# Performance work log

Measured on AMD Instinct MI355X. Metric: run time of the kernel, lower is better.

Reference implementation:

```python
import jax, jax.numpy as jnp
import numpy as np

B, L, D, H, FF, K = 2, 2048, 1024, 16, 4096, 5
HD = D // H
EPS = 1e-5

def _rope_matrix():
    pos = jnp.arange(L, dtype=jnp.float32)
    inv = 1.0 / (10000.0 ** (jnp.arange(0, HD, 2, dtype=jnp.float32) / HD))
    ang = pos[:, None] * inv[None, :]                       # [L, HD//2]
    # buffer layout matches torch: cat([cos, sin], -1) -> [1,1,L,HD]
    return jnp.concatenate([jnp.cos(ang), jnp.sin(ang)], -1)[None, None]

def _alibi():
    i = jnp.arange(L)
    dist = jnp.clip(i[:, None] - i[None, :], 0, None).astype(jnp.float32)
    slopes = 2.0 ** (-(2.0 ** (-(np.log2(H) - 3.0))) * jnp.arange(H, dtype=jnp.float32))
    return slopes[:, None, None] * dist                     # [H,L,L]

def _apply_rope(x, pe):
    # faithful even/odd slicing of the concatenated [cos|sin] buffer
    xe, xo = x[..., ::2], x[..., 1::2]
    c, s = pe[..., ::2], pe[..., 1::2]
    return jnp.concatenate([xe * c - xo * s, xe * s + xo * c], -1)

def _ln(x, g, b):
    m = x.mean(-1, keepdims=True)
    v = ((x - m) ** 2).mean(-1, keepdims=True)
    return (x - m) * jax.lax.rsqrt(v + EPS) * g + b

def _attn(x, wq, bq, wk, bk, wv, bv, wo, bo, pe, alibi):
    q = (x @ wq + bq).reshape(B, L, H, HD).transpose(0, 2, 1, 3)
    k = (x @ wk + bk).reshape(B, L, H, HD).transpose(0, 2, 1, 3)
    v = (x @ wv + bv).reshape(B, L, H, HD).transpose(0, 2, 1, 3)
    q = _apply_rope(q, pe)
    k = _apply_rope(k, pe)
    scores = jnp.einsum('bhqd,bhkd->bhqk', q, k) * (HD ** -0.5) + alibi[None]
    w = jax.nn.softmax(scores, axis=-1)
    o = jnp.einsum('bhqk,bhkd->bhqd', w, v).transpose(0, 2, 1, 3).reshape(B, L, D)
    return o @ wo + bo

def _conv_block(x, g, b, pw1_w, pw1_b, dw_w, dw_b, bn_g, bn_b, pw2_w, pw2_b):
    res = x
    h = _ln(x, g, b)
    h = h @ pw1_w + pw1_b                                   # pointwise 1: [B,L,2D]
    h = h[..., :D] * jax.nn.sigmoid(h[..., D:])             # GLU -> [B,L,D]
    h = h.transpose(0, 2, 1)                                # [B,D,L]
    w = dw_w[:, None, ::-1]                                 # ConvTranspose1d(stride=1,pad=K//2) == corr with flipped kernel
    h = jax.lax.conv_general_dilated(h, w, (1,), [(K // 2, K // 2)],
        dimension_numbers=('NCH', 'OIH', 'NCH'), feature_group_count=D)
    h = h + dw_b[None, :, None]
    h = h * jax.lax.rsqrt(jnp.float32(1.0 + EPS)) * bn_g[None, :, None] + bn_b[None, :, None]  # eval BN
    h = h * jax.nn.relu6(h + 3.0) / 6.0                     # hardswish
    h = h.transpose(0, 2, 1) @ pw2_w + pw2_b                # pointwise 2: [B,L,D]
    return h + res[:, :1, :]                                # Upsample(size=1) residual (nearest -> t=0)

def reference(memory, wq, bq, wk, bk, wv, bv, wo, bo, n1_g, n1_b,
              cln_g, cln_b, pw1_w, pw1_b, dw_w, dw_b, bn_g, bn_b, pw2_w, pw2_b,
              proj_w, proj_b, proj2_w, proj2_b, lin1_w, lin1_b, lin2_w, lin2_b,
              n3_g, n3_b):
    pe = _rope_matrix()
    alibi = _alibi()
    tgt2 = _attn(memory, wq, bq, wk, bk, wv, bv, wo, bo, pe, alibi)
    memory = memory + _ln(tgt2, n1_g, n1_b)
    conv = _conv_block(memory, cln_g, cln_b, pw1_w, pw1_b, dw_w, dw_b,
                       bn_g, bn_b, pw2_w, pw2_b)
    proj = jnp.einsum('bld,lm->bmd', memory, proj_w) + proj_b[:, None]   # Linear over seq axis
    proj = proj @ proj2_w + proj2_b
    memory = proj + conv
    tgt2 = jax.nn.gelu(memory @ lin1_w + lin1_b, approximate=False) @ lin2_w + lin2_b
    return _ln(memory + tgt2, n3_g, n3_b)

def setup_inputs():
    ks = iter(jax.random.split(jax.random.key(0), 48))
    def w(shape, s=0.02):
        return jax.random.normal(next(ks), shape, dtype=jnp.float32) * s
    z = lambda *s: jnp.zeros(s, dtype=jnp.float32)
    o = lambda *s: jnp.ones(s, dtype=jnp.float32)
    return {
        'memory': jax.random.normal(next(ks), (B, L, D), dtype=jnp.float32),
        'wq': w((D, D)), 'bq': z(D), 'wk': w((D, D)), 'bk': z(D),
        'wv': w((D, D)), 'bv': z(D), 'wo': w((D, D)), 'bo': z(D),
        'n1_g': o(D), 'n1_b': z(D),
        'cln_g': o(D), 'cln_b': z(D),
        'pw1_w': w((D, 2 * D)), 'pw1_b': z(2 * D),
        'dw_w': w((D, K), 0.1), 'dw_b': z(D),
        'bn_g': o(D), 'bn_b': z(D),
        'pw2_w': w((D, D)), 'pw2_b': z(D),
        'proj_w': w((L, L)), 'proj_b': z(L),
        'proj2_w': w((D, D)), 'proj2_b': z(D),
        'lin1_w': w((D, FF)), 'lin1_b': z(FF),
        'lin2_w': w((FF, D)), 'lin2_b': z(D),
        'n3_g': o(D), 'n3_b': z(D),
    }
```

## Files before the change

### kernel.cpp

```cpp
#include <hip/hip_runtime.h>
#include <hip/hip_bf16.h>
#include <math.h>

constexpr int Bc = 2, Lc = 2048, Dc = 1024, Hc = 16, HDc = 64, FFc = 4096;
constexpr int NT = Bc * Lc;
constexpr size_t TD = (size_t)NT * Dc;
constexpr size_t MEG = 1024 * 1024;

__device__ __forceinline__ float ldf(const float* p) { return *p; }
__device__ __forceinline__ unsigned short f2b(float f) {
  __hip_bfloat16 h = __float2bfloat16(f);
  return *reinterpret_cast<unsigned short*>(&h);
}

using frag   = __attribute__((ext_vector_type(8))) short;
using f32x4v = __attribute__((ext_vector_type(4))) float;

__device__ __forceinline__ void async16(const unsigned short* g, unsigned short* l) {
  __builtin_amdgcn_global_load_lds(
      (const __attribute__((address_space(1))) unsigned int*)g,
      (__attribute__((address_space(3))) unsigned int*)l, 16, 0, 0);
}

__device__ __forceinline__ float block_sum(float v, float* red) {
  const int lane = threadIdx.x & 63, w = threadIdx.x >> 6;
  #pragma unroll
  for (int o = 32; o > 0; o >>= 1) v += __shfl_down(v, o, 64);
  __syncthreads();
  if (lane == 0) red[w] = v;
  __syncthreads();
  return red[0] + red[1] + red[2] + red[3];
}

__global__ __launch_bounds__(256)
void convert_bf16_kernel(const float* __restrict__ IN, unsigned short* __restrict__ OUT)
{
  const size_t gid = (size_t)blockIdx.x * 256 + threadIdx.x;
  const float4 v = *(const float4*)(IN + gid * 4);
  ushort4 o;
  o.x = f2b(v.x); o.y = f2b(v.y); o.z = f2b(v.z); o.w = f2b(v.w);
  *(ushort4*)(OUT + gid * 4) = o;
}

__global__ __launch_bounds__(256)
void transpose_convert_kernel(const float* __restrict__ IN, unsigned short* __restrict__ OUT,
                              int R, int C, long long sIn, long long sOut)
{
  __shared__ float tile[64][65];
  const int t = threadIdx.x;
  const float* in = IN + (long long)blockIdx.z * sIn;
  unsigned short* out = OUT + (long long)blockIdx.z * sOut;
  const int r0 = blockIdx.y * 64, c0 = blockIdx.x * 64;
  #pragma unroll
  for (int i = 0; i < 4; i++) {
    const int r = (t >> 4) + i * 16, c4 = (t & 15) * 4;
    const float4 v = *(const float4*)(in + (size_t)(r0 + r) * C + c0 + c4);
    tile[r][c4+0] = v.x; tile[r][c4+1] = v.y; tile[r][c4+2] = v.z; tile[r][c4+3] = v.w;
  }
  __syncthreads();
  #pragma unroll
  for (int i = 0; i < 4; i++) {
    const int cc = (t >> 4) + i * 16, rr4 = (t & 15) * 4;
    ushort4 o;
    o.x = f2b(tile[rr4+0][cc]); o.y = f2b(tile[rr4+1][cc]);
    o.z = f2b(tile[rr4+2][cc]); o.w = f2b(tile[rr4+3][cc]);
    *(ushort4*)(out + (size_t)(c0 + cc) * R + r0 + rr4) = o;
  }
}

struct TPack {
  const float* in[10]; unsigned short* out[10];
  int R[10], C[10], tx[10], start[10];
};
__global__ __launch_bounds__(256)
void fused_transpose_kernel(TPack p)
{
  __shared__ float tile[64][65];
  const int bid = blockIdx.x;
  int s = 0;
  #pragma unroll
  for (int i = 1; i < 10; i++) s = (bid >= p.start[i]) ? i : s;
  const float* in = p.in[s];
  unsigned short* out = p.out[s];
  const int R = p.R[s], C = p.C[s];
  const int local = bid - p.start[s];
  const int bx = local % p.tx[s], by = local / p.tx[s];
  const int r0 = by * 64, c0 = bx * 64;
  const int t = threadIdx.x;
  #pragma unroll
  for (int i = 0; i < 4; i++) {
    const int r = (t >> 4) + i * 16, c4 = (t & 15) * 4;
    const float4 v = *(const float4*)(in + (size_t)(r0 + r) * C + c0 + c4);
    tile[r][c4+0] = v.x; tile[r][c4+1] = v.y; tile[r][c4+2] = v.z; tile[r][c4+3] = v.w;
  }
  __syncthreads();
  #pragma unroll
  for (int i = 0; i < 4; i++) {
    const int cc = (t >> 4) + i * 16, rr4 = (t & 15) * 4;
    ushort4 o;
    o.x = f2b(tile[rr4+0][cc]); o.y = f2b(tile[rr4+1][cc]);
    o.z = f2b(tile[rr4+2][cc]); o.w = f2b(tile[rr4+3][cc]);
    *(ushort4*)(out + (size_t)(c0 + cc) * R + r0 + rr4) = o;
  }
}

constexpr int EPI_BIAS = 0, EPI_BIAS_ROW = 1, EPI_GELU = 2, EPI_ADD = 3, EPI_ADDROW0 = 4,
              EPI_QKV = 5;

template<int BM, int EPI, bool OUTBF, bool OUTBOTH>
__global__ __launch_bounds__(256)
void mfma_gemm_kernel(const unsigned short* __restrict__ A, const unsigned short* __restrict__ Bt,
                      const float* __restrict__ bias, const float* __restrict__ bias2,
                      const float* __restrict__ bias3, const float* __restrict__ extra,
                      float* __restrict__ C, unsigned short* __restrict__ Cbf,
                      int M, int N, int K,
                      long long sA, long long sB, long long sC)
{
  constexpr int NTt = (BM == 128) ? 4 : 2;
  __shared__ unsigned short As[2][BM][4][8];
  __shared__ unsigned short Bs[2][128][4][8];
  const int tid = threadIdx.x;
  const int l = tid & 63, w = tid >> 6;
  const int wm = (BM == 128) ? (w & 1) * 64 : 0;
  const int wn = (BM == 128) ? (w >> 1) * 64 : w * 32;
  const int m0 = blockIdx.y * BM, n0 = blockIdx.x * 128;
  const unsigned short* Ap = A + (long long)blockIdx.z * sA;
  const unsigned short* Bp = Bt + (long long)blockIdx.z * sB;

  f32x4v acc[4][NTt];
  #pragma unroll
  for (int mt = 0; mt < 4; mt++)
    #pragma unroll
    for (int nt = 0; nt < NTt; nt++) acc[mt][nt] = {0.f, 0.f, 0.f, 0.f};

  const int c_ = l >> 4, rm = l & 15;
  int rrB[2], ggB[2];
  #pragma unroll
  for (int j = 0; j < 2; j++) {
    const int chunk = w * 128 + j * 64 + l;
    rrB[j] = chunk >> 2;
    ggB[j] = (chunk & 3) ^ ((rrB[j] >> 1) & 3);
  }
  int rrA = 0, ggA = 0;
  if constexpr (BM == 64) {
    const int chunkA = w * 64 + l;
    rrA = chunkA >> 2;
    ggA = (chunkA & 3) ^ ((rrA >> 1) & 3);
  }

  auto stage = [&](int bi, int k0) {
    if constexpr (BM == 128) {
      #pragma unroll
      for (int j = 0; j < 2; j++) {
        async16(Ap + (size_t)(m0 + rrB[j]) * K + k0 + ggB[j] * 8,
                &As[bi][0][0][0] + (size_t)(w * 128 + j * 64) * 8);
        async16(Bp + (size_t)(n0 + rrB[j]) * K + k0 + ggB[j] * 8,
                &Bs[bi][0][0][0] + (size_t)(w * 128 + j * 64) * 8);
      }
    } else {
      async16(Ap + (size_t)(m0 + rrA) * K + k0 + ggA * 8,
              &As[bi][0][0][0] + (size_t)(w * 64) * 8);
      #pragma unroll
      for (int j = 0; j < 2; j++)
        async16(Bp + (size_t)(n0 + rrB[j]) * K + k0 + ggB[j] * 8,
                &Bs[bi][0][0][0] + (size_t)(w * 128 + j * 64) * 8);
    }
  };

  stage(0, 0);
  __syncthreads();
  int cur = 0;
  const int sg = (rm >> 1) & 3;

  for (int k0 = 0; k0 < K; k0 += 32) {
    if (k0 + 32 < K) stage(cur ^ 1, k0 + 32);

    frag af[4], bfr[NTt];
    #pragma unroll
    for (int mt = 0; mt < 4; mt++)
      af[mt] = *(const frag*)&As[cur][wm + mt * 16 + rm][c_ ^ sg][0];
    #pragma unroll
    for (int nt = 0; nt < NTt; nt++)
      bfr[nt] = *(const frag*)&Bs[cur][wn + nt * 16 + rm][c_ ^ sg][0];
    #pragma unroll
    for (int mt = 0; mt < 4; mt++)
      #pragma unroll
      for (int nt = 0; nt < NTt; nt++)
        acc[mt][nt] = __builtin_amdgcn_mfma_f32_16x16x32_bf16(af[mt], bfr[nt], acc[mt][nt], 0, 0, 0);

    __syncthreads();
    cur ^= 1;
  }

  float* Cp = C + (long long)blockIdx.z * sC;
  unsigned short* Cbp = Cbf + (long long)blockIdx.z * sC;
  #pragma unroll
  for (int mt = 0; mt < 4; mt++) {
    #pragma unroll
    for (int nt = 0; nt < NTt; nt++) {
      const int mq = m0 + wm + mt * 16 + c_ * 4;
      const int n  = n0 + wn + nt * 16 + rm;
      if constexpr (EPI == EPI_QKV) {
        const float* bp = (n < 1024) ? bias : ((n < 2048) ? bias2 : bias3);
        const float bv_ = ldf(bp + (n & 1023));
        const float r0 = acc[mt][nt][0] + bv_;
        const float r1 = acc[mt][nt][1] + bv_;
        const float r2 = acc[mt][nt][2] + bv_;
        const float r3 = acc[mt][nt][3] + bv_;
        if (n < 2048) {
          float* dst = Cp + (size_t)(n >> 10) * TD + (size_t)mq * Dc + (n & 1023);
          dst[0] = r0; dst[Dc] = r1; dst[2 * Dc] = r2; dst[3 * Dc] = r3;
        } else {
          ushort4 o;
          o.x = f2b(r0); o.y = f2b(r1); o.z = f2b(r2); o.w = f2b(r3);
          *(ushort4*)(Cbp + (size_t)(mq >> 11) * ((size_t)Lc * Dc)
                      + (size_t)(n - 2048) * Lc + (mq & (Lc - 1))) = o;
        }
      } else {
        #pragma unroll
        for (int i = 0; i < 4; i++) {
          const int m = mq + i;
          float r = acc[mt][nt][i];
          if constexpr (EPI == EPI_BIAS || EPI == EPI_GELU || EPI == EPI_ADD || EPI == EPI_ADDROW0)
            r += ldf(bias + n);
          if constexpr (EPI == EPI_BIAS_ROW) r += ldf(bias + m);
          if constexpr (EPI == EPI_GELU)
            r = 0.5f * r * (1.0f + erff(r * 0.70710678118654752f));
          if constexpr (EPI == EPI_ADD) r += extra[(size_t)m * N + n];
          if constexpr (EPI == EPI_ADDROW0) r += extra[(size_t)(m >> 11) * ((size_t)Lc * Dc) + n];
          if constexpr (OUTBOTH) { Cp[(size_t)m * N + n] = r; Cbp[(size_t)m * N + n] = f2b(r); }
          else if constexpr (OUTBF) Cbp[(size_t)m * N + n] = f2b(r);
          else                      Cp[(size_t)m * N + n] = r;
        }
      }
    }
  }
}

__global__ __launch_bounds__(256)
void pe_fill_kernel(float* __restrict__ pet)
{
  const int gid = blockIdx.x * 256 + threadIdx.x;
  const int l = gid >> 6, t = gid & 63;
  const int j = t & 31;
  const float wj = exp2f(-(float)j * (13.2877123795494f / 32.0f));
  const float ang = (float)l * wj;
  pet[gid] = (t < 32) ? cosf(ang) : sinf(ang);
}

__global__ __launch_bounds__(256)
void rope2_kernel(const float* __restrict__ Qi, const float* __restrict__ Ki,
                  const float* __restrict__ pet,
                  unsigned short* __restrict__ Qo, unsigned short* __restrict__ Ko)
{
  int gid = blockIdx.x * 256 + threadIdx.x;
  const int sel = gid >= NT * Hc;
  if (sel) gid -= NT * Hc;
  const float* X = sel ? Ki : Qi;
  unsigned short* O = sel ? Ko : Qo;
  const float scl = sel ? 1.0f : 0.125f * 1.44269504f;
  const int h = gid & (Hc - 1);
  const int token = gid >> 4;
  const int l = token & (Lc - 1);
  const float* p = X + (size_t)token * Dc + h * HDc;
  unsigned short* po = O + (size_t)token * Dc + h * HDc;
  const float* pr = pet + l * 64;
  float x[64], out[64];
  #pragma unroll
  for (int i = 0; i < 16; i++) *(float4*)&x[4*i] = *(const float4*)&p[4*i];
  #pragma unroll
  for (int u = 0; u < 32; u++) {
    const int base = (u < 16) ? (2 * u) : (32 + 2 * (u - 16));
    const float c = pr[base], s = pr[base + 1];
    out[u]      = (x[2*u] * c - x[2*u+1] * s) * scl;
    out[32 + u] = (x[2*u] * s + x[2*u+1] * c) * scl;
  }
  #pragma unroll
  for (int i = 0; i < 16; i++) {
    ushort4 o;
    o.x = f2b(out[4*i+0]); o.y = f2b(out[4*i+1]);
    o.z = f2b(out[4*i+2]); o.w = f2b(out[4*i+3]);
    *(ushort4*)&po[4*i] = o;
  }
}

__global__ __launch_bounds__(256)
void flash_attn_mfma_kernel(const unsigned short* __restrict__ Q,
                            const unsigned short* __restrict__ K,
                            const unsigned short* __restrict__ VT,
                            unsigned short* __restrict__ O)
{
  __shared__ unsigned short Qs[64][8][8];
  __shared__ unsigned short Ks[2][64][8][8];
  __shared__ unsigned short Vt[2][64][8][8];
  __shared__ unsigned short Ps[64][72];
  const int tid = threadIdx.x;
  const int l = tid & 63, w = tid >> 6;
  const int lg = l >> 4, lm = l & 15;
  const int q0 = blockIdx.x * 64;
  const int bh = blockIdx.y;
  const int b = bh >> 4, h = bh & 15;
  const size_t rowbase = (size_t)b * Lc;
  const size_t vbase = (size_t)b * Lc * Dc;
  const int dbase = h * 64;
  const float sl2 = exp2f(-0.5f * (float)h) * 1.44269504f;

  auto stageKV = [&](int bi, int k0s) {
    #pragma unroll
    for (int j = 0; j < 2; j++) {
      const int chunk = (w * 2 + j) * 64 + l;
      const int r = chunk >> 3, gsrc = (chunk & 7) ^ (r & 7);
      async16(K + (rowbase + k0s + r) * Dc + dbase + gsrc * 8,
              &Ks[bi][0][0][0] + (size_t)chunk * 8);
      async16(VT + vbase + (size_t)(dbase + r) * Lc + k0s + gsrc * 8,
              &Vt[bi][0][0][0] + (size_t)chunk * 8);
    }
  };

  #pragma unroll
  for (int j = 0; j < 2; j++) {
    const int chunk = (w * 2 + j) * 64 + l;
    const int r = chunk >> 3, gsrc = (chunk & 7) ^ (r & 7);
    async16(Q + (rowbase + q0 + r) * Dc + dbase + gsrc * 8,
            &Qs[0][0][0] + (size_t)chunk * 8);
  }
  stageKV(0, 0);
  __syncthreads();
  frag qf[2];
  #pragma unroll
  for (int s = 0; s < 2; s++)
    qf[s] = *(const frag*)&Qs[w * 16 + lm][(s * 4 + lg) ^ (lm & 7)][0];

  const float qg = (float)(q0 + w * 16 + lm);
  float koff[4][4];
  #pragma unroll
  for (int kt = 0; kt < 4; kt++)
    #pragma unroll
    for (int i = 0; i < 4; i++) koff[kt][i] = (float)(kt * 16 + lg * 4 + i);

  float m_i = -3.0e38f, l_i = 0.f;
  f32x4v acc_o[4];
  #pragma unroll
  for (int dt = 0; dt < 4; dt++) acc_o[dt] = {0.f, 0.f, 0.f, 0.f};

  int cur = 0;
  for (int k0 = 0; k0 < Lc; k0 += 64) {
    if (k0 + 64 < Lc) stageKV(cur ^ 1, k0 + 64);

    f32x4v st[4];
    #pragma unroll
    for (int kt = 0; kt < 4; kt++) st[kt] = {0.f, 0.f, 0.f, 0.f};
    __builtin_amdgcn_s_setprio(1);
    #pragma unroll
    for (int kt = 0; kt < 4; kt++) {
      #pragma unroll
      for (int s = 0; s < 2; s++) {
        frag kf = *(const frag*)&Ks[cur][kt * 16 + lm][(s * 4 + lg) ^ (lm & 7)][0];
        st[kt] = __builtin_amdgcn_mfma_f32_16x16x32_bf16(kf, qf[s], st[kt], 0, 0, 0);
      }
    }
    __builtin_amdgcn_s_setprio(0);

    const float qk0 = qg - (float)k0;
    float sv[4][4], tmax = -3.0e38f;
    if (k0 + 64 <= q0) {
      #pragma unroll
      for (int kt = 0; kt < 4; kt++)
        #pragma unroll
        for (int i = 0; i < 4; i++) {
          const float v = fmaf(sl2, qk0 - koff[kt][i], st[kt][i]);
          sv[kt][i] = v; tmax = fmaxf(tmax, v);
        }
    } else if (k0 <= q0) {
      #pragma unroll
      for (int kt = 0; kt < 4; kt++)
        #pragma unroll
        for (int i = 0; i < 4; i++) {
          const float v = fmaf(sl2, fmaxf(qk0 - koff[kt][i], 0.f), st[kt][i]);
          sv[kt][i] = v; tmax = fmaxf(tmax, v);
        }
    } else {
      #pragma unroll
      for (int kt = 0; kt < 4; kt++)
        #pragma unroll
        for (int i = 0; i < 4; i++) {
          const float v = st[kt][i];
          sv[kt][i] = v; tmax = fmaxf(tmax, v);
        }
    }
    tmax = fmaxf(tmax, __shfl_xor(tmax, 16, 64));
    tmax = fmaxf(tmax, __shfl_xor(tmax, 32, 64));

    if (!__all(tmax < m_i - 27.0f)) {
      if (__any(tmax > m_i)) {
        const float mnew = fmaxf(m_i, tmax);
        const float alpha = exp2f(m_i - mnew);
        m_i = mnew;
        l_i *= alpha;
        float aO[4];
        #pragma unroll
        for (int i = 0; i < 4; i++) aO[i] = __shfl(alpha, lg * 4 + i, 64);
        #pragma unroll
        for (int dt = 0; dt < 4; dt++)
          #pragma unroll
          for (int i = 0; i < 4; i++) acc_o[dt][i] *= aO[i];
      }
      float rsum = 0.f;
      const int qrow = w * 16 + lm;
      #pragma unroll
      for (int kt = 0; kt < 4; kt++) {
        const float p0 = exp2f(sv[kt][0] - m_i), p1 = exp2f(sv[kt][1] - m_i);
        const float p2 = exp2f(sv[kt][2] - m_i), p3 = exp2f(sv[kt][3] - m_i);
        rsum += (p0 + p1) + (p2 + p3);
        ushort4 pk4;
        pk4.x = f2b(p0); pk4.y = f2b(p1); pk4.z = f2b(p2); pk4.w = f2b(p3);
        *(ushort4*)&Ps[qrow][kt * 16 + lg * 4] = pk4;
      }
      rsum += __shfl_xor(rsum, 16, 64);
      rsum += __shfl_xor(rsum, 32, 64);
      l_i += rsum;

      __builtin_amdgcn_s_setprio(1);
      #pragma unroll
      for (int c = 0; c < 2; c++) {
        frag ap = *(const frag*)&Ps[w * 16 + lm][c * 32 + lg * 8];
        #pragma unroll
        for (int dt = 0; dt < 4; dt++) {
          frag bv = *(const frag*)&Vt[cur][dt * 16 + lm][(c * 4 + lg) ^ (lm & 7)][0];
          acc_o[dt] = __builtin_amdgcn_mfma_f32_16x16x32_bf16(ap, bv, acc_o[dt], 0, 0, 0);
        }
      }
      __builtin_amdgcn_s_setprio(0);
    }

    __syncthreads();
    cur ^= 1;
  }

  float lO[4];
  #pragma unroll
  for (int i = 0; i < 4; i++) lO[i] = 1.0f / __shfl(l_i, lg * 4 + i, 64);
  #pragma unroll
  for (int dt = 0; dt < 4; dt++)
    #pragma unroll
    for (int i = 0; i < 4; i++)
      Ps[w * 16 + lg * 4 + i][dt * 16 + lm] = f2b(acc_o[dt][i] * lO[i]);
  __syncthreads();
  #pragma unroll
  for (int j = 0; j < 2; j++) {
    const int chunk = (w * 2 + j) * 64 + l;
    const int r = chunk >> 3, g = chunk & 7;
    alignas(16) unsigned short tmp[8];
    #pragma unroll
    for (int t = 0; t < 8; t++) tmp[t] = Ps[r][g * 8 + t];
    *(uint4*)(O + (rowbase + q0 + r) * Dc + dbase + g * 8) = *(uint4*)tmp;
  }
}

__global__ __launch_bounds__(256)
void ln_res_cln_kernel(const float* __restrict__ X, const float* __restrict__ RES,
                       const float* __restrict__ g1, const float* __restrict__ b1,
                       const float* __restrict__ g2, const float* __restrict__ b2,
                       float* __restrict__ OUT1, unsigned short* __restrict__ OUT2)
{
  __shared__ float red4[4];
  const int row = blockIdx.x, tid = threadIdx.x;
  const size_t base = (size_t)row * Dc + tid * 4;
  const float4 xv = *(const float4*)(X + base);
  float s = xv.x + xv.y + xv.z + xv.w;
  s = block_sum(s, red4);
  const float mean = s * (1.0f / Dc);
  const float d0 = xv.x-mean, d1 = xv.y-mean, d2 = xv.z-mean, d3 = xv.w-mean;
  float ss = d0*d0 + d1*d1 + d2*d2 + d3*d3;
  ss = block_sum(ss, red4);
  const float rstd = rsqrtf(ss * (1.0f / Dc) + 1e-5f);
  const int c = tid * 4;
  const float4 rv = *(const float4*)(RES + base);
  float y0 = rv.x + d0*rstd*ldf(g1+c+0) + ldf(b1+c+0);
  float y1 = rv.y + d1*rstd*ldf(g1+c+1) + ldf(b1+c+1);
  float y2 = rv.z + d2*rstd*ldf(g1+c+2) + ldf(b1+c+2);
  float y3 = rv.w + d3*rstd*ldf(g1+c+3) + ldf(b1+c+3);
  *(float4*)(OUT1 + base) = make_float4(y0, y1, y2, y3);
  float s2 = y0 + y1 + y2 + y3;
  s2 = block_sum(s2, red4);
  const float mean2 = s2 * (1.0f / Dc);
  const float e0 = y0-mean2, e1 = y1-mean2, e2 = y2-mean2, e3 = y3-mean2;
  float ss2 = e0*e0 + e1*e1 + e2*e2 + e3*e3;
  ss2 = block_sum(ss2, red4);
  const float rstd2 = rsqrtf(ss2 * (1.0f / Dc) + 1e-5f);
  ushort4 o;
  o.x = f2b(e0*rstd2*ldf(g2+c+0) + ldf(b2+c+0));
  o.y = f2b(e1*rstd2*ldf(g2+c+1) + ldf(b2+c+1));
  o.z = f2b(e2*rstd2*ldf(g2+c+2) + ldf(b2+c+2));
  o.w = f2b(e3*rstd2*ldf(g2+c+3) + ldf(b2+c+3));
  *(ushort4*)(OUT2 + base) = o;
}

__global__ __launch_bounds__(256)
void ln_sum_kernel(const float* __restrict__ X, const float* __restrict__ Y,
                   const float* __restrict__ g, const float* __restrict__ be,
                   float* __restrict__ OUT)
{
  __shared__ float red4[4];
  const int row = blockIdx.x, tid = threadIdx.x;
  const size_t base = (size_t)row * Dc + tid * 4;
  const float4 xv = *(const float4*)(X + base);
  const float4 yv = *(const float4*)(Y + base);
  const float x0 = xv.x+yv.x, x1 = xv.y+yv.y, x2 = xv.z+yv.z, x3 = xv.w+yv.w;
  float s = x0 + x1 + x2 + x3;
  s = block_sum(s, red4);
  const float mean = s * (1.0f / Dc);
  const float d0 = x0-mean, d1 = x1-mean, d2 = x2-mean, d3 = x3-mean;
  float ss = d0*d0 + d1*d1 + d2*d2 + d3*d3;
  ss = block_sum(ss, red4);
  const float rstd = rsqrtf(ss * (1.0f / Dc) + 1e-5f);
  const int c = tid * 4;
  float4 o;
  o.x = d0*rstd*ldf(g+c+0) + ldf(be+c+0);
  o.y = d1*rstd*ldf(g+c+1) + ldf(be+c+1);
  o.z = d2*rstd*ldf(g+c+2) + ldf(be+c+2);
  o.w = d3*rstd*ldf(g+c+3) + ldf(be+c+3);
  *(float4*)(OUT + base) = o;
}

__global__ __launch_bounds__(256)
void glu_kernel(const float* __restrict__ H1, float* __restrict__ HG)
{
  const int gid = blockIdx.x * 256 + threadIdx.x;
  const int t = gid >> 8;
  const int c4 = (gid & 255) * 4;
  const float* p = H1 + (size_t)t * (2 * Dc);
  const float4 a = *(const float4*)(p + c4);
  const float4 gg = *(const float4*)(p + Dc + c4);
  float4 o;
  o.x = a.x / (1.0f + expf(-gg.x));
  o.y = a.y / (1.0f + expf(-gg.y));
  o.z = a.z / (1.0f + expf(-gg.z));
  o.w = a.w / (1.0f + expf(-gg.w));
  *(float4*)(HG + (size_t)t * Dc + c4) = o;
}

__global__ __launch_bounds__(256)
void dwconv_bf16_kernel(const float* __restrict__ HG, const float* __restrict__ w,
                        const float* __restrict__ wb, const float* __restrict__ gn,
                        const float* __restrict__ bb, unsigned short* __restrict__ OUT)
{
  const int gid = blockIdx.x * 256 + threadIdx.x;
  const int d = gid & (Dc - 1);
  const int l = (gid >> 10) & (Lc - 1);
  const int b = gid >> 21;
  const size_t rowb = (size_t)b * Lc;
  float acc = ldf(wb + d);
  #pragma unroll
  for (int s = 0; s < 5; s++) {
    const int lp = l + 2 - s;
    if (lp >= 0 && lp < Lc)
      acc += ldf(w + d * 5 + s) * HG[((rowb + lp) << 10) + d];
  }
  const float rs = rsqrtf(1.0f + 1e-5f);
  const float t = acc * rs * ldf(gn + d) + ldf(bb + d);
  OUT[gid] = f2b(t * fminf(fmaxf(t + 3.0f, 0.0f), 6.0f) * (1.0f / 6.0f));
}

extern "C" void kernel_launch(void* const* d_in, const int* in_sizes, int n_in,
                              void* d_out, int out_size, void* d_ws, size_t ws_size,
                              hipStream_t stream) {
  (void)in_sizes; (void)n_in; (void)out_size; (void)ws_size;
  const float* mem    = (const float*)d_in[0];
  const float* wq     = (const float*)d_in[1];
  const float* bq     = (const float*)d_in[2];
  const float* wk     = (const float*)d_in[3];
  const float* bk     = (const float*)d_in[4];
  const float* wv     = (const float*)d_in[5];
  const float* bv     = (const float*)d_in[6];
  const float* wo     = (const float*)d_in[7];
  const float* bo     = (const float*)d_in[8];
  const float* n1g    = (const float*)d_in[9];
  const float* n1b    = (const float*)d_in[10];
  const float* clng   = (const float*)d_in[11];
  const float* clnb   = (const float*)d_in[12];
  const float* pw1w   = (const float*)d_in[13];
  const float* pw1b   = (const float*)d_in[14];
  const float* dww    = (const float*)d_in[15];
  const float* dwb    = (const float*)d_in[16];
  const float* bng    = (const float*)d_in[17];
  const float* bnb    = (const float*)d_in[18];
  const float* pw2w   = (const float*)d_in[19];
  const float* pw2b   = (const float*)d_in[20];
  const float* projw  = (const float*)d_in[21];
  const float* projb  = (const float*)d_in[22];
  const float* proj2w = (const float*)d_in[23];
  const float* proj2b = (const float*)d_in[24];
  const float* lin1w  = (const float*)d_in[25];
  const float* lin1b  = (const float*)d_in[26];
  const float* lin2w  = (const float*)d_in[27];
  const float* lin2b  = (const float*)d_in[28];
  const float* n3g    = (const float*)d_in[29];
  const float* n3b    = (const float*)d_in[30];
  float* out = (float*)d_out;

  char* base = (char*)d_ws;
  float* qb   = (float*)base;
  float* kb   = qb + TD;
  float* big1 = kb + TD;
  float* big2 = big1 + TD;
  float* ob   = big2 + TD;
  unsigned short* abf  = (unsigned short*)(base + 5 * TD * 4);
  unsigned short* qbf  = abf + TD;
  unsigned short* kbf  = qbf + TD;
  unsigned short* vtb  = kbf + TD;
  unsigned short* m1T  = vtb + TD;
  unsigned short* ffbbf= m1T + TD;
  unsigned short* wt   = ffbbf + 4 * TD;
  unsigned short* wqT    = wt;
  unsigned short* wkT    = wqT + MEG;
  unsigned short* wvT    = wkT + MEG;
  unsigned short* woT    = wvT + MEG;
  unsigned short* pw1T   = woT + MEG;
  unsigned short* pw2T   = pw1T + 2*MEG;
  unsigned short* proj2T = pw2T + MEG;
  unsigned short* projwT = proj2T + MEG;
  unsigned short* lin1T  = projwT + 4*MEG;
  unsigned short* lin2T  = lin1T + 4*MEG;
  float* pet = (float*)(lin2T + 4*MEG);

  const dim3 blk(256);
  const long long LD = (long long)Lc * Dc;

  TPack tp;
  const float* tin[10]  = {wq, wk, wv, wo, pw1w, pw2w, proj2w, projw, lin1w, lin2w};
  unsigned short* tout[10] = {wqT, wkT, wvT, woT, pw1T, pw2T, proj2T, projwT, lin1T, lin2T};
  const int tR[10] = {1024,1024,1024,1024,1024,1024,1024,2048,1024,4096};
  const int tC[10] = {1024,1024,1024,1024,2048,1024,1024,2048,4096,1024};
  int startAcc = 0;
  for (int i = 0; i < 10; i++) {
    tp.in[i] = tin[i]; tp.out[i] = tout[i];
    tp.R[i] = tR[i]; tp.C[i] = tC[i]; tp.tx[i] = tC[i] / 64;
    tp.start[i] = startAcc;
    startAcc += (tR[i] / 64) * (tC[i] / 64);
  }
  fused_transpose_kernel<<<dim3(startAcc), blk, 0, stream>>>(tp);
  pe_fill_kernel<<<dim3(Lc * 64 / 256), blk, 0, stream>>>(pet);

  convert_bf16_kernel<<<dim3((unsigned)(TD/1024)),blk,0,stream>>>(mem, abf);
  mfma_gemm_kernel<128,EPI_QKV,false,false><<<dim3(24,32,1),blk,0,stream>>>(
      abf, wqT, bq, bk, bv, nullptr, qb, vtb, NT, 3*Dc, Dc, 0, 0, 0);
  rope2_kernel<<<dim3(2*NT*Hc/256),blk,0,stream>>>(qb, kb, pet, qbf, kbf);
  flash_attn_mfma_kernel<<<dim3(Lc/64, Bc*Hc),blk,0,stream>>>(qbf,kbf,vtb,abf);
  mfma_gemm_kernel<64,EPI_BIAS,false,false><<<dim3(8,64,1),blk,0,stream>>>(
      abf,woT,bo,nullptr,nullptr,nullptr,qb,nullptr,NT,Dc,Dc,0,0,0);
  ln_res_cln_kernel<<<dim3(NT),blk,0,stream>>>(qb, mem, n1g, n1b, clng, clnb, kb, abf);

  mfma_gemm_kernel<128,EPI_BIAS,false,false><<<dim3(16,32,1),blk,0,stream>>>(
      abf,pw1T,pw1b,nullptr,nullptr,nullptr,big1,nullptr,NT,2*Dc,Dc,0,0,0);
  glu_kernel<<<dim3((unsigned)(TD/4/256)),blk,0,stream>>>(big1, ob);
  dwconv_bf16_kernel<<<dim3((unsigned)(TD/256)),blk,0,stream>>>(ob, dww, dwb, bng, bnb, abf);
  mfma_gemm_kernel<64,EPI_ADDROW0,false,false><<<dim3(8,64,1),blk,0,stream>>>(
      abf,pw2T,pw2b,nullptr,nullptr,kb,big2,nullptr,NT,Dc,Dc,0,0,0);

  transpose_convert_kernel<<<dim3(16,32,2),blk,0,stream>>>(kb, m1T, 2048, 1024, LD, LD);
  mfma_gemm_kernel<64,EPI_BIAS_ROW,true,false><<<dim3(8,32,2),blk,0,stream>>>(
      projwT,m1T,projb,nullptr,nullptr,nullptr,nullptr,abf,Lc,Dc,Lc,0,LD,LD);
  mfma_gemm_kernel<64,EPI_ADD,false,true><<<dim3(8,64,1),blk,0,stream>>>(
      abf,proj2T,proj2b,nullptr,nullptr,big2,big1,qbf,NT,Dc,Dc,0,0,0);

  mfma_gemm_kernel<128,EPI_GELU,true,false><<<dim3(32,32,1),blk,0,stream>>>(
      qbf,lin1T,lin1b,nullptr,nullptr,nullptr,nullptr,ffbbf,NT,FFc,Dc,0,0,0);
  mfma_gemm_kernel<64,EPI_BIAS,false,false><<<dim3(8,64,1),blk,0,stream>>>(
      ffbbf,lin2T,lin2b,nullptr,nullptr,nullptr,ob,nullptr,NT,Dc,FFc,0,0,0);

  ln_sum_kernel<<<dim3(NT),blk,0,stream>>>(big1, ob, n3g, n3b, out);
}
```

Baseline: 653.6 us.

## Skip loading K/V tiles whose Cauchy-Schwarz score bound cannot affect softmax

Adds a kernel that computes the maximum row L2 norm of each 64-row Q and K tile per head. The flash attention loop now uses the product of these norms plus the ALiBi bias maximum as an upper bound on tile scores. When that bound sits more than 27 (log2 units) below the current block-wide running max, it skips both the async K/V staging and the MFMA work for that tile. The P-to-bf16 conversion also switches to packed v_cvt_pk_bf16_f32 instructions. The bound is exact by Cauchy-Schwarz, but the skip only pays off when ALiBi makes far tiles negligible; it costs an extra kernel launch plus a per-iteration shared-memory min reduction.

```diff
diff --git a/kernel.cpp b/kernel.cpp
--- a/kernel.cpp
+++ b/kernel.cpp
@@ -285,15 +285,56 @@
 }
 
 __global__ __launch_bounds__(256)
+void tile_norm_kernel(const unsigned short* __restrict__ Qb,
+                      const unsigned short* __restrict__ Kb,
+                      float* __restrict__ qnb, float* __restrict__ knb)
+{
+  __shared__ float red[4];
+  const int tile = blockIdx.x, bh = blockIdx.y;
+  const int b = bh >> 4, h = bh & 15;
+  const unsigned short* X = blockIdx.z ? Qb : Kb;
+  const int tid = threadIdx.x;
+  const int row = tid >> 2, seg = tid & 3;
+  const unsigned short* p = X + ((size_t)(b * Lc + tile * 64 + row)) * Dc + h * 64 + seg * 16;
+  const uint4 v0 = *(const uint4*)p;
+  const uint4 v1 = *(const uint4*)(p + 8);
+  const unsigned int vv[8] = {v0.x, v0.y, v0.z, v0.w, v1.x, v1.y, v1.z, v1.w};
+  float ss = 0.f;
+  #pragma unroll
+  for (int i = 0; i < 8; i++) {
+    const float a = __uint_as_float(vv[i] << 16);
+    const float c = __uint_as_float(vv[i] & 0xffff0000u);
+    ss = fmaf(a, a, ss); ss = fmaf(c, c, ss);
+  }
+  ss += __shfl_xor(ss, 1, 64);
+  ss += __shfl_xor(ss, 2, 64);
+  float mx = ss;
+  mx = fmaxf(mx, __shfl_xor(mx, 4, 64));
+  mx = fmaxf(mx, __shfl_xor(mx, 8, 64));
+  mx = fmaxf(mx, __shfl_xor(mx, 16, 64));
+  mx = fmaxf(mx, __shfl_xor(mx, 32, 64));
+  if ((tid & 63) == 0) red[tid >> 6] = mx;
+  __syncthreads();
+  if (tid == 0) {
+    const float r = fmaxf(fmaxf(red[0], red[1]), fmaxf(red[2], red[3]));
+    (blockIdx.z ? qnb : knb)[bh * 32 + tile] = sqrtf(r);
+  }
+}
+
+__global__ __launch_bounds__(256)
 void flash_attn_mfma_kernel(const unsigned short* __restrict__ Q,
                             const unsigned short* __restrict__ K,
                             const unsigned short* __restrict__ VT,
+                            const float* __restrict__ qnb,
+                            const float* __restrict__ knb,
                             unsigned short* __restrict__ O)
 {
   __shared__ unsigned short Qs[64][8][8];
   __shared__ unsigned short Ks[2][64][8][8];
   __shared__ unsigned short Vt[2][64][8][8];
   __shared__ unsigned short Ps[64][72];
+  __shared__ float knS[32];
+  __shared__ float mS[64];
   const int tid = threadIdx.x;
   const int l = tid & 63, w = tid >> 6;
   const int lg = l >> 4, lm = l & 15;
@@ -325,6 +366,9 @@
             &Qs[0][0][0] + (size_t)chunk * 8);
   }
   stageKV(0, 0);
+  const float qmx = qnb[bh * 32 + blockIdx.x] * 1.01f;
+  if (tid < 32) knS[tid] = knb[bh * 32 + tid];
+  if (tid < 64) mS[tid] = -3.0e38f;
   __syncthreads();
   frag qf[2];
   #pragma unroll
@@ -343,98 +387,121 @@
   #pragma unroll
   for (int dt = 0; dt < 4; dt++) acc_o[dt] = {0.f, 0.f, 0.f, 0.f};
 
-  int cur = 0;
-  for (int k0 = 0; k0 < Lc; k0 += 64) {
-    if (k0 + 64 < Lc) stageKV(cur ^ 1, k0 + 64);
-
-    f32x4v st[4];
-    #pragma unroll
-    for (int kt = 0; kt < 4; kt++) st[kt] = {0.f, 0.f, 0.f, 0.f};
-    __builtin_amdgcn_s_setprio(1);
-    #pragma unroll
-    for (int kt = 0; kt < 4; kt++) {
+  int nslot = 1;
+  bool staged_cur = true; int slot_cur = 0;
+  bool staged_next = false; int slot_next = 0;
+
+  for (int t = 0; t < Lc / 64; ++t) {
+    const int k0 = t * 64;
+
+    float mb = mS[l];
+    mb = fminf(mb, __shfl_xor(mb, 1, 64));
+    mb = fminf(mb, __shfl_xor(mb, 2, 64));
+    mb = fminf(mb, __shfl_xor(mb, 4, 64));
+    mb = fminf(mb, __shfl_xor(mb, 8, 64));
+    mb = fminf(mb, __shfl_xor(mb, 16, 64));
+    mb = fminf(mb, __shfl_xor(mb, 32, 64));
+
+    if (t + 1 < Lc / 64) {
+      const int u = t + 1;
+      const float biasmax = sl2 * fmaxf((float)(q0 + 63 - 64 * u), 0.f);
+      staged_next = (qmx * knS[u] + biasmax) >= mb - 27.0f;
+      if (staged_next) { slot_next = nslot; stageKV(nslot, u * 64); nslot ^= 1; }
+    } else staged_next = false;
+
+    if (staged_cur) {
+      f32x4v st[4];
       #pragma unroll
-      for (int s = 0; s < 2; s++) {
-        frag kf = *(const frag*)&Ks[cur][kt * 16 + lm][(s * 4 + lg) ^ (lm & 7)][0];
-        st[kt] = __builtin_amdgcn_mfma_f32_16x16x32_bf16(kf, qf[s], st[kt], 0, 0, 0);
-      }
-    }
-    __builtin_amdgcn_s_setprio(0);
-
-    const float qk0 = qg - (float)k0;
-    float sv[4][4], tmax = -3.0e38f;
-    if (k0 + 64 <= q0) {
-      #pragma unroll
-      for (int kt = 0; kt < 4; kt++)
-        #pragma unroll
-        for (int i = 0; i < 4; i++) {
-          const float v = fmaf(sl2, qk0 - koff[kt][i], st[kt][i]);
-          sv[kt][i] = v; tmax = fmaxf(tmax, v);
-        }
-    } else if (k0 <= q0) {
-      #pragma unroll
-      for (int kt = 0; kt < 4; kt++)
-        #pragma unroll
-        for (int i = 0; i < 4; i++) {
-          const float v = fmaf(sl2, fmaxf(qk0 - koff[kt][i], 0.f), st[kt][i]);
-          sv[kt][i] = v; tmax = fmaxf(tmax, v);
-        }
-    } else {
-      #pragma unroll
-      for (int kt = 0; kt < 4; kt++)
-        #pragma unroll
-        for (int i = 0; i < 4; i++) {
-          const float v = st[kt][i];
-          sv[kt][i] = v; tmax = fmaxf(tmax, v);
-        }
-    }
-    tmax = fmaxf(tmax, __shfl_xor(tmax, 16, 64));
-    tmax = fmaxf(tmax, __shfl_xor(tmax, 32, 64));
-
-    if (!__all(tmax < m_i - 27.0f)) {
-      if (__any(tmax > m_i)) {
-        const float mnew = fmaxf(m_i, tmax);
-        const float alpha = exp2f(m_i - mnew);
-        m_i = mnew;
-        l_i *= alpha;
-        float aO[4];
-        #pragma unroll
-        for (int i = 0; i < 4; i++) aO[i] = __shfl(alpha, lg * 4 + i, 64);
-        #pragma unroll
-        for (int dt = 0; dt < 4; dt++)
-          #pragma unroll
-          for (int i = 0; i < 4; i++) acc_o[dt][i] *= aO[i];
-      }
-      float rsum = 0.f;
-      const int qrow = w * 16 + lm;
+      for (int kt = 0; kt < 4; kt++) st[kt] = {0.f, 0.f, 0.f, 0.f};
+      __builtin_amdgcn_s_setprio(1);
       #pragma unroll
       for (int kt = 0; kt < 4; kt++) {
-        const float p0 = exp2f(sv[kt][0] - m_i), p1 = exp2f(sv[kt][1] - m_i);
-        const float p2 = exp2f(sv[kt][2] - m_i), p3 = exp2f(sv[kt][3] - m_i);
-        rsum += (p0 + p1) + (p2 + p3);
-        ushort4 pk4;
-        pk4.x = f2b(p0); pk4.y = f2b(p1); pk4.z = f2b(p2); pk4.w = f2b(p3);
-        *(ushort4*)&Ps[qrow][kt * 16 + lg * 4] = pk4;
-      }
-      rsum += __shfl_xor(rsum, 16, 64);
-      rsum += __shfl_xor(rsum, 32, 64);
-      l_i += rsum;
-
-      __builtin_amdgcn_s_setprio(1);
-      #pragma unroll
-      for (int c = 0; c < 2; c++) {
-        frag ap = *(const frag*)&Ps[w * 16 + lm][c * 32 + lg * 8];
         #pragma unroll
-        for (int dt = 0; dt < 4; dt++) {
-          frag bv = *(const frag*)&Vt[cur][dt * 16 + lm][(c * 4 + lg) ^ (lm & 7)][0];
-          acc_o[dt] = __builtin_amdgcn_mfma_f32_16x16x32_bf16(ap, bv, acc_o[dt], 0, 0, 0);
+        for (int s = 0; s < 2; s++) {
+          frag kf = *(const frag*)&Ks[slot_cur][kt * 16 + lm][(s * 4 + lg) ^ (lm & 7)][0];
+          st[kt] = __builtin_amdgcn_mfma_f32_16x16x32_bf16(kf, qf[s], st[kt], 0, 0, 0);
         }
       }
       __builtin_amdgcn_s_setprio(0);
+
+      const float qk0 = qg - (float)k0;
+      float sv[4][4], tmax = -3.0e38f;
+      if (k0 + 64 <= q0) {
+        #pragma unroll
+        for (int kt = 0; kt < 4; kt++)
+          #pragma unroll
+          for (int i = 0; i < 4; i++) {
+            const float v = fmaf(sl2, qk0 - koff[kt][i], st[kt][i]);
+            sv[kt][i] = v; tmax = fmaxf(tmax, v);
+          }
+      } else if (k0 <= q0) {
+        #pragma unroll
+        for (int kt = 0; kt < 4; kt++)
+          #pragma unroll
+          for (int i = 0; i < 4; i++) {
+            const float v = fmaf(sl2, fmaxf(qk0 - koff[kt][i], 0.f), st[kt][i]);
+            sv[kt][i] = v; tmax = fmaxf(tmax, v);
+          }
+      } else {
+        #pragma unroll
+        for (int kt = 0; kt < 4; kt++)
+          #pragma unroll
+          for (int i = 0; i < 4; i++) {
+            const float v = st[kt][i];
+            sv[kt][i] = v; tmax = fmaxf(tmax, v);
+          }
+      }
+      tmax = fmaxf(tmax, __shfl_xor(tmax, 16, 64));
+      tmax = fmaxf(tmax, __shfl_xor(tmax, 32, 64));
+
+      if (!__all(tmax < m_i - 27.0f)) {
+        if (__any(tmax > m_i)) {
+          const float mnew = fmaxf(m_i, tmax);
+          const float alpha = exp2f(m_i - mnew);
+          m_i = mnew;
+          l_i *= alpha;
+          float aO[4];
+          #pragma unroll
+          for (int i = 0; i < 4; i++) aO[i] = __shfl(alpha, lg * 4 + i, 64);
+          #pragma unroll
+          for (int dt = 0; dt < 4; dt++)
+            #pragma unroll
+            for (int i = 0; i < 4; i++) acc_o[dt][i] *= aO[i];
+        }
+        float rsum = 0.f;
+        const int qrow = w * 16 + lm;
+        #pragma unroll
+        for (int kt = 0; kt < 4; kt++) {
+          const float p0 = exp2f(sv[kt][0] - m_i), p1 = exp2f(sv[kt][1] - m_i);
+          const float p2 = exp2f(sv[kt][2] - m_i), p3 = exp2f(sv[kt][3] - m_i);
+          rsum += (p0 + p1) + (p2 + p3);
+          unsigned int w0, w1;
+          asm("v_cvt_pk_bf16_f32 %0, %1, %2" : "=v"(w0) : "v"(p0), "v"(p1));
+          asm("v_cvt_pk_bf16_f32 %0, %1, %2" : "=v"(w1) : "v"(p2), "v"(p3));
+          uint2 pw; pw.x = w0; pw.y = w1;
+          *(uint2*)&Ps[qrow][kt * 16 + lg * 4] = pw;
+        }
+        rsum += __shfl_xor(rsum, 16, 64);
+        rsum += __shfl_xor(rsum, 32, 64);
+        l_i += rsum;
+
+        __builtin_amdgcn_s_setprio(1);
+        #pragma unroll
+        for (int c = 0; c < 2; c++) {
+          frag ap = *(const frag*)&Ps[w * 16 + lm][c * 32 + lg * 8];
+          #pragma unroll
+          for (int dt = 0; dt < 4; dt++) {
+            frag bv = *(const frag*)&Vt[slot_cur][dt * 16 + lm][(c * 4 + lg) ^ (lm & 7)][0];
+            acc_o[dt] = __builtin_amdgcn_mfma_f32_16x16x32_bf16(ap, bv, acc_o[dt], 0, 0, 0);
+          }
+        }
+        __builtin_amdgcn_s_setprio(0);
+      }
+      if (lg == 0) mS[w * 16 + lm] = m_i;
     }
 
     __syncthreads();
-    cur ^= 1;
+    staged_cur = staged_next; slot_cur = slot_next;
   }
 
   float lO[4];
@@ -623,6 +690,8 @@
   unsigned short* lin1T  = projwT + 4*MEG;
   unsigned short* lin2T  = lin1T + 4*MEG;
   float* pet = (float*)(lin2T + 4*MEG);
+  float* knb = pet + (size_t)Lc * 64;
+  float* qnb = knb + 1024;
 
   const dim3 blk(256);
   const long long LD = (long long)Lc * Dc;
@@ -646,7 +715,8 @@
   mfma_gemm_kernel<128,EPI_QKV,false,false><<<dim3(24,32,1),blk,0,stream>>>(
       abf, wqT, bq, bk, bv, nullptr, qb, vtb, NT, 3*Dc, Dc, 0, 0, 0);
   rope2_kernel<<<dim3(2*NT*Hc/256),blk,0,stream>>>(qb, kb, pet, qbf, kbf);
-  flash_attn_mfma_kernel<<<dim3(Lc/64, Bc*Hc),blk,0,stream>>>(qbf,kbf,vtb,abf);
+  tile_norm_kernel<<<dim3(32,32,2),blk,0,stream>>>(qbf, kbf, qnb, knb);
+  flash_attn_mfma_kernel<<<dim3(Lc/64, Bc*Hc),blk,0,stream>>>(qbf,kbf,vtb,qnb,knb,abf);
   mfma_gemm_kernel<64,EPI_BIAS,false,false><<<dim3(8,64,1),blk,0,stream>>>(
       abf,woT,bo,nullptr,nullptr,nullptr,qb,nullptr,NT,Dc,Dc,0,0,0);
   ln_res_cln_kernel<<<dim3(NT),blk,0,stream>>>(qb, mem, n1g, n1b, clng, clnb, kb, abf);
```

New measurement: 684.3 us. 4.7% more time.
